# Kernel tuning notes

Measured on AMD Instinct MI355X. Metric: run time of the kernel, lower is better.

The kernel has to match this reference:

```python
import jax, jax.numpy as jnp
import numpy as np

B, L, D = 2, 2048, 4096
H, KV, HD = 32, 8, 128          # query heads, kv heads, head_dim
G = H // KV                      # GQA group size
THETA = 10000.0
SCALE = HD ** -0.5


def apply_rope(x, offset=0):
    """Non-traditional (half-split) RoPE. x: [B, heads, L, HD]."""
    hd = x.shape[-1]
    half = hd // 2
    inv_freq = 1.0 / (THETA ** (jnp.arange(0, hd, 2, dtype=jnp.float32) / hd))  # [half]
    pos = jnp.arange(offset, offset + x.shape[2], dtype=jnp.float32)            # [L]
    ang = pos[:, None] * inv_freq[None, :]                                      # [L, half]
    cos = jnp.cos(ang).astype(x.dtype)
    sin = jnp.sin(ang).astype(x.dtype)
    x1, x2 = x[..., :half], x[..., half:]
    return jnp.concatenate([x1 * cos - x2 * sin, x2 * cos + x1 * sin], axis=-1)


def setup_inputs() -> dict:
    key = jax.random.key(0)
    ks = jax.random.split(key, 8)
    s = 0.02
    return {
        "x": jax.random.normal(ks[0], (B, L, D), dtype=jnp.float32),
        "Wq": jax.random.normal(ks[1], (D, H * HD), dtype=jnp.float32) * s,
        "bq": jnp.zeros((H * HD,), dtype=jnp.float32),
        "Wk": jax.random.normal(ks[2], (D, KV * HD), dtype=jnp.float32) * s,
        "bk": jnp.zeros((KV * HD,), dtype=jnp.float32),
        "Wv": jax.random.normal(ks[3], (D, KV * HD), dtype=jnp.float32) * s,
        "bv": jnp.zeros((KV * HD,), dtype=jnp.float32),
        "Wo": jax.random.normal(ks[4], (H * HD, D), dtype=jnp.float32) * s,
    }


def reference(x, Wq, bq, Wk, bk, Wv, bv, Wo):
    b, l, _ = x.shape
    # projections
    q = (x @ Wq + bq).reshape(b, l, H, HD).transpose(0, 2, 1, 3)   # [B,H,L,HD]
    k = (x @ Wk + bk).reshape(b, l, KV, HD).transpose(0, 2, 1, 3)  # [B,KV,L,HD]
    v = (x @ Wv + bv).reshape(b, l, KV, HD).transpose(0, 2, 1, 3)  # [B,KV,L,HD]
    # RoPE (cache=None path, offset 0)
    q = apply_rope(q)
    k = apply_rope(k)
    # GQA SDPA without materializing repeated KV heads
    qg = q.reshape(b, KV, G, l, HD)                                 # [B,KV,G,L,HD]
    scores = jnp.einsum('bkgld,bkmd->bkglm', qg, k) * SCALE         # [B,KV,G,L,L]
    probs = jax.nn.softmax(scores, axis=-1)
    out = jnp.einsum('bkglm,bkmd->bkgld', probs, v)                 # [B,KV,G,L,HD]
    out = out.reshape(b, H, l, HD).transpose(0, 2, 1, 3).reshape(b, l, H * HD)
    return out @ Wo
```

## Files before the change

kernel.cpp:

```cpp
#include <hip/hip_runtime.h>
#include <stdint.h>
#include <stddef.h>


typedef _Float16 half_t;
typedef __attribute__((ext_vector_type(4))) _Float16 f16x4;
typedef __attribute__((ext_vector_type(8))) _Float16 f16x8;
typedef __attribute__((ext_vector_type(4))) float f32x4;

#define NB 2
#define NL 2048
#define ND 4096
#define NH 32
#define NKV 8
#define NHD 128
#define NG 4
#define NQKV 6144
#define QK_SCALE 0.08838834764831845f
#define RLOG2E 1.4426950408889634f
#define M0 6.0f
#define THR 8.0f

static __device__ __forceinline__ void gll16(const void* g, void* l) {
  __builtin_amdgcn_global_load_lds(
      (__attribute__((address_space(1))) void*)(void*)(g),
      (__attribute__((address_space(3))) void*)(l),
      16, 0, 0);
}

__global__ void convert_f32_f16_kernel(const float* __restrict__ in,
                                       half_t* __restrict__ out, int n4) {
  int i = blockIdx.x * 256 + threadIdx.x;
  if (i >= n4) return;
  const float4 v = reinterpret_cast<const float4*>(in)[i];
  f16x4 o;
  o[0] = (half_t)v.x; o[1] = (half_t)v.y; o[2] = (half_t)v.z; o[3] = (half_t)v.w;
  reinterpret_cast<f16x4*>(out)[i] = o;
}

__global__ void wtrans_kernel(const float* __restrict__ W,
                              half_t* __restrict__ Wt, int K, int N) {
  __shared__ float tile[32][33];
  const int n0 = blockIdx.x * 32;
  const int k0 = blockIdx.y * 32;
  const int tx = threadIdx.x, ty = threadIdx.y;
#pragma unroll
  for (int r = 0; r < 32; r += 8)
    tile[ty + r][tx] = W[(size_t)(k0 + ty + r) * N + n0 + tx];
  __syncthreads();
#pragma unroll
  for (int r = 0; r < 32; r += 8)
    Wt[(size_t)(n0 + ty + r) * K + k0 + tx] = (half_t)tile[tx][ty + r];
}

template <typename OutT>
__global__ __launch_bounds__(512, 2) void gemm256_kernel(
    const half_t* __restrict__ A, const half_t* __restrict__ Bt,
    const float* __restrict__ B0, const float* __restrict__ B1,
    const float* __restrict__ B2, OutT* __restrict__ C,
    int M, int N, int K) {
  constexpr int BK = 32;
  __shared__ __align__(16) half_t As[4][256 * BK];
  __shared__ __align__(16) half_t Bs[4][256 * BK];

  const int tid = threadIdx.x;
  const int wave = tid >> 6, lane = tid & 63;
  const int r16 = lane & 15, quad = lane >> 4;
  const int wm = wave >> 2, wn = wave & 3;

  const int nbx = N >> 8;
  const int lid = (int)(blockIdx.y * gridDim.x + blockIdx.x);
  const int nwg = (int)(gridDim.x * gridDim.y);
  const int cpx = nwg >> 3;
  const int swz = (lid & 7) * cpx + (lid >> 3);
  const int brow = (swz / nbx) * 256;
  const int bcol = (swz % nbx) * 256;

  const int NT = K >> 5;

  auto stageA = [&](int t) {
    const int buf = t & 3;
    const int k0 = t << 5;
#pragma unroll
    for (int j = 0; j < 2; ++j) {
      const int s = j * 512 + wave * 64 + lane;
      const int row = s >> 2;
      const int cg = (s & 3) ^ (row & 3);
      gll16(A + (size_t)(brow + row) * K + k0 + cg * 8,
            &As[buf][(j * 512 + wave * 64) * 8]);
    }
  };
  auto stageB = [&](int t) {
    const int buf = t & 3;
    const int k0 = t << 5;
#pragma unroll
    for (int j = 0; j < 2; ++j) {
      const int s = j * 512 + wave * 64 + lane;
      const int row = s >> 2;
      const int cg = (s & 3) ^ (row & 3);
      gll16(Bt + (size_t)(bcol + row) * K + k0 + cg * 8,
            &Bs[buf][(j * 512 + wave * 64) * 8]);
    }
  };

  f32x4 acc[8][4] = {};
  const int csw = (quad ^ (r16 & 3)) << 3;

  stageA(0); stageB(0); stageA(1); stageB(1); stageA(2); stageB(2);
  asm volatile("s_waitcnt vmcnt(8)" ::: "memory");
  __builtin_amdgcn_s_barrier();

  for (int t = 0; t < NT; ++t) {
    const int buf = t & 3;
    const half_t* Ab = &As[buf][0];
    const half_t* Bb = &Bs[buf][0];

    f16x8 af[4], bf[4];
#pragma unroll
    for (int ni = 0; ni < 4; ++ni)
      bf[ni] = *reinterpret_cast<const f16x8*>(
          &Bb[(wn * 64 + ni * 16 + r16) * BK + csw]);
#pragma unroll
    for (int mi = 0; mi < 4; ++mi)
      af[mi] = *reinterpret_cast<const f16x8*>(
          &Ab[(wm * 128 + mi * 16 + r16) * BK + csw]);
    if (t + 3 < NT) stageA(t + 3);
    __builtin_amdgcn_sched_barrier(0);
    __builtin_amdgcn_s_barrier();
    asm volatile("s_waitcnt lgkmcnt(0)" ::: "memory");
    __builtin_amdgcn_sched_barrier(0);
    __builtin_amdgcn_s_setprio(1);
#pragma unroll
    for (int mi = 0; mi < 4; ++mi)
#pragma unroll
      for (int ni = 0; ni < 4; ++ni)
        acc[mi][ni] = __builtin_amdgcn_mfma_f32_16x16x32_f16(
            af[mi], bf[ni], acc[mi][ni], 0, 0, 0);
    __builtin_amdgcn_s_setprio(0);
    __builtin_amdgcn_s_barrier();

    f16x8 ah[4];
#pragma unroll
    for (int mi = 0; mi < 4; ++mi)
      ah[mi] = *reinterpret_cast<const f16x8*>(
          &Ab[(wm * 128 + 64 + mi * 16 + r16) * BK + csw]);
    if (t + 3 < NT) stageB(t + 3);
    if (t + 3 < NT) {
      asm volatile("s_waitcnt vmcnt(8)" ::: "memory");
    } else if (t + 2 < NT) {
      asm volatile("s_waitcnt vmcnt(4)" ::: "memory");
    } else if (t + 1 < NT) {
      asm volatile("s_waitcnt vmcnt(0)" ::: "memory");
    }
    __builtin_amdgcn_sched_barrier(0);
    __builtin_amdgcn_s_barrier();
    asm volatile("s_waitcnt lgkmcnt(0)" ::: "memory");
    __builtin_amdgcn_sched_barrier(0);
    __builtin_amdgcn_s_setprio(1);
#pragma unroll
    for (int mi = 0; mi < 4; ++mi)
#pragma unroll
      for (int ni = 0; ni < 4; ++ni)
        acc[mi + 4][ni] = __builtin_amdgcn_mfma_f32_16x16x32_f16(
            ah[mi], bf[ni], acc[mi + 4][ni], 0, 0, 0);
    __builtin_amdgcn_s_setprio(0);
    __builtin_amdgcn_s_barrier();
  }

#pragma unroll
  for (int ni = 0; ni < 4; ++ni) {
    const int col = bcol + wn * 64 + ni * 16 + r16;
    float bv = 0.0f;
    if (B0) bv = (col < ND) ? B0[col]
                            : (col < ND + NKV * NHD ? B1[col - ND]
                                                    : B2[col - ND - NKV * NHD]);
#pragma unroll
    for (int mi = 0; mi < 8; ++mi) {
      const int row0 = brow + wm * 128 + mi * 16 + quad * 4;
#pragma unroll
      for (int i = 0; i < 4; ++i)
        C[(size_t)(row0 + i) * N + col] = (OutT)(acc[mi][ni][i] + bv);
    }
  }
}

__global__ void ropepack_kernel(const half_t* __restrict__ rawh,
                                half_t* __restrict__ qb,
                                half_t* __restrict__ kb) {
  const size_t idx = (size_t)blockIdx.x * 256 + threadIdx.x;
  const int d = (int)(idx & 63);
  size_t t = idx >> 6;
  const int hp = (int)(t % (NH + NKV)); t /= (NH + NKV);
  const int l = (int)(t % NL);
  const int b = (int)(t / NL);
  const bool isQ = hp < NH;
  const int col0 = isQ ? hp * NHD : ND + (hp - NH) * NHD;
  const half_t* src = rawh + ((size_t)b * NL + l) * NQKV + col0;
  const float x1 = (float)src[d];
  const float x2 = (float)src[d + 64];
  const float inv_freq = exp2f(-(float)d * 0.20762050593045935f);
  const float ang = (float)l * inv_freq;
  float sn, cs;
  __sincosf(ang, &sn, &cs);
  const float scale = isQ ? QK_SCALE : 1.0f;
  half_t* dst = isQ ? qb + ((size_t)(b * NH + hp) * NL + l) * NHD
                    : kb + ((size_t)(b * NKV + (hp - NH)) * NL + l) * NHD;
  dst[d]      = (half_t)((x1 * cs - x2 * sn) * scale);
  dst[d + 64] = (half_t)((x2 * cs + x1 * sn) * scale);
}

__global__ void vtrans16_kernel(const half_t* __restrict__ rawh,
                                half_t* __restrict__ Vt) {
  __shared__ half_t tile[32][34];
  const int bkv = blockIdx.z;
  const int l0 = blockIdx.x * 32;
  const int d0 = blockIdx.y * 32;
  const int b = bkv / NKV, kvh = bkv % NKV;
  const int tx = threadIdx.x, ty = threadIdx.y;
#pragma unroll
  for (int r = 0; r < 32; r += 8)
    tile[ty + r][tx] = rawh[(size_t)(b * NL + l0 + ty + r) * NQKV
                            + ND + NKV * NHD + kvh * NHD + d0 + tx];
  __syncthreads();
  half_t* dst = Vt + (size_t)bkv * NHD * NL;
#pragma unroll
  for (int r = 0; r < 32; r += 8)
    dst[(size_t)(d0 + ty + r) * NL + l0 + tx] = tile[tx][ty + r];
}

#define KVB 64

__global__ __launch_bounds__(512, 2) void attn_kernel(
    const half_t* __restrict__ Q,
    const half_t* __restrict__ Kh,
    const half_t* __restrict__ Vt,
    half_t* __restrict__ O) {
  __shared__ half_t Ks[2][KVB * NHD];
  __shared__ half_t Vs[2][NHD * KVB];
  __shared__ half_t Ps[8][16 * 64];

  const int tid = threadIdx.x;
  const int wave = tid >> 6, lane = tid & 63;
  const int r16 = lane & 15, quad = lane >> 4;
  const int r7 = r16 & 7;

  const int bid = (int)blockIdx.x;
  const int swz = (bid & 7) * 64 + (bid >> 3);
  const int nqt = NL / 256;
  const int bh = swz / nqt, qt = swz % nqt;
  const int b = bh / NH, h = bh % NH;
  const int kvh = h / NG;

  const int qrow0 = qt * 256 + wave * 32;
  const half_t* Qb = Q  + ((size_t)(b * NH + h) * NL + qrow0) * NHD;
  const half_t* Kb = Kh + ((size_t)(b * NKV + kvh) * NL) * NHD;
  const half_t* Vb = Vt + ((size_t)(b * NKV + kvh) * NHD) * NL;
  half_t* Pw = &Ps[wave][0];

  auto stage = [&](int buf, int n0) {
#pragma unroll
    for (int j = 0; j < 2; ++j) {
      const int slot = j * 512 + wave * 64 + lane;
      {
        const int row = slot >> 4;
        const int c = (slot & 15) ^ (row & 7);
        gll16(Kb + (size_t)(n0 + row) * NHD + c * 8,
              &Ks[buf][(j * 512 + wave * 64) * 8]);
      }
      {
        const int row = slot >> 3;
        const int c = (slot & 7) ^ (row & 7);
        gll16(Vb + (size_t)row * NL + n0 + c * 8,
              &Vs[buf][(j * 512 + wave * 64) * 8]);
      }
    }
  };

  stage(0, 0);

  f16x8 qf[2][4];
#pragma unroll
  for (int rt = 0; rt < 2; ++rt)
#pragma unroll
    for (int c = 0; c < 4; ++c)
      qf[rt][c] = *reinterpret_cast<const f16x8*>(
          &Qb[(size_t)(rt * 16 + r16) * NHD + c * 32 + quad * 8]);

  f32x4 oacc[2][8];
  float m_run[2][4], lsum[2][4];
#pragma unroll
  for (int rt = 0; rt < 2; ++rt) {
#pragma unroll
    for (int i = 0; i < 4; ++i) { m_run[rt][i] = M0; lsum[rt][i] = 0.0f; }
#pragma unroll
    for (int dt = 0; dt < 8; ++dt) oacc[rt][dt] = (f32x4){0.f, 0.f, 0.f, 0.f};
  }

  const int swzread = r7 ^ ((r16 >> 3) * 5);

  asm volatile("s_waitcnt vmcnt(0)" ::: "memory");
  __syncthreads();

  int cur = 0;
  for (int t = 0; t < NL / KVB; ++t, cur ^= 1) {
    if (t + 1 < NL / KVB) stage(cur ^ 1, (t + 1) * KVB);

    const half_t* Kc = &Ks[cur][0];
    const half_t* Vc = &Vs[cur][0];

    f32x4 s[2][4] = {};
#pragma unroll
    for (int c = 0; c < 4; ++c) {
      const int ch = ((c * 4 + quad) ^ r7) * 8;
#pragma unroll
      for (int nt = 0; nt < 4; ++nt) {
        f16x8 kf = *reinterpret_cast<const f16x8*>(&Kc[(nt * 16 + r16) * NHD + ch]);
        s[0][nt] = __builtin_amdgcn_mfma_f32_16x16x32_f16(qf[0][c], kf, s[0][nt], 0, 0, 0);
        s[1][nt] = __builtin_amdgcn_mfma_f32_16x16x32_f16(qf[1][c], kf, s[1][nt], 0, 0, 0);
      }
    }

    float mx[2][4];
    bool need = false;
#pragma unroll
    for (int rt = 0; rt < 2; ++rt)
#pragma unroll
      for (int i = 0; i < 4; ++i) {
        mx[rt][i] = fmaxf(fmaxf(s[rt][0][i], s[rt][1][i]),
                          fmaxf(s[rt][2][i], s[rt][3][i]));
        need = need || (mx[rt][i] > m_run[rt][i] + THR);
      }
    if (__any(need ? 1 : 0)) {
#pragma unroll
      for (int rt = 0; rt < 2; ++rt)
#pragma unroll
        for (int i = 0; i < 4; ++i) {
          float m = mx[rt][i];
#pragma unroll
          for (int off = 1; off < 16; off <<= 1)
            m = fmaxf(m, __shfl_xor(m, off));
          const float mn = fmaxf(m_run[rt][i], m);
          const float corr = exp2f((m_run[rt][i] - mn) * RLOG2E);
          m_run[rt][i] = mn;
          lsum[rt][i] *= corr;
#pragma unroll
          for (int dt = 0; dt < 8; ++dt) oacc[rt][dt][i] *= corr;
        }
    }

    f16x8 pa[2][2];
#pragma unroll
    for (int rt = 0; rt < 2; ++rt) {
#pragma unroll
      for (int i = 0; i < 4; ++i) {
        const float mrl = m_run[rt][i] * RLOG2E;
        float p[4];
#pragma unroll
        for (int nt = 0; nt < 4; ++nt)
          p[nt] = exp2f(s[rt][nt][i] * RLOG2E - mrl);
        lsum[rt][i] += (p[0] + p[1]) + (p[2] + p[3]);
        const int row = quad * 4 + i;
        const int swzr = (row & 7) ^ ((row >> 3) * 5);
#pragma unroll
        for (int nt = 0; nt < 4; ++nt)
          Pw[row * 64 + (((nt * 2 + (r16 >> 3)) ^ swzr) * 8) + r7] = (half_t)p[nt];
      }
      pa[rt][0] = *reinterpret_cast<const f16x8*>(&Pw[r16 * 64 + ((quad ^ swzread) * 8)]);
      pa[rt][1] = *reinterpret_cast<const f16x8*>(&Pw[r16 * 64 + (((4 + quad) ^ swzread) * 8)]);
    }

    const int ch0 = (quad ^ r7) * 8;
    const int ch1 = ((4 + quad) ^ r7) * 8;
#pragma unroll
    for (int dt = 0; dt < 8; ++dt) {
      const int row = dt * 16 + r16;
      f16x8 v0 = *reinterpret_cast<const f16x8*>(&Vc[row * 64 + ch0]);
      f16x8 v1 = *reinterpret_cast<const f16x8*>(&Vc[row * 64 + ch1]);
      oacc[0][dt] = __builtin_amdgcn_mfma_f32_16x16x32_f16(pa[0][0], v0, oacc[0][dt], 0, 0, 0);
      oacc[0][dt] = __builtin_amdgcn_mfma_f32_16x16x32_f16(pa[0][1], v1, oacc[0][dt], 0, 0, 0);
      oacc[1][dt] = __builtin_amdgcn_mfma_f32_16x16x32_f16(pa[1][0], v0, oacc[1][dt], 0, 0, 0);
      oacc[1][dt] = __builtin_amdgcn_mfma_f32_16x16x32_f16(pa[1][1], v1, oacc[1][dt], 0, 0, 0);
    }

    asm volatile("s_waitcnt vmcnt(0)" ::: "memory");
    __syncthreads();
  }

  half_t* Ob = O + ((size_t)(b * NL) + qrow0) * (NH * NHD) + (size_t)h * NHD;
#pragma unroll
  for (int rt = 0; rt < 2; ++rt)
#pragma unroll
    for (int i = 0; i < 4; ++i) {
      float l = lsum[rt][i];
#pragma unroll
      for (int off = 1; off < 16; off <<= 1)
        l += __shfl_xor(l, off);
      const float inv = 1.0f / l;
      const int rl = rt * 16 + quad * 4 + i;
#pragma unroll
      for (int dt = 0; dt < 8; ++dt)
        Ob[(size_t)rl * (NH * NHD) + dt * 16 + r16] =
            (half_t)(oacc[rt][dt][i] * inv);
    }
}

extern "C" void kernel_launch(void* const* d_in, const int* in_sizes, int n_in,
                              void* d_out, int out_size, void* d_ws, size_t ws_size,
                              hipStream_t stream) {
  const float* x  = (const float*)d_in[0];
  const float* Wq = (const float*)d_in[1];
  const float* bq = (const float*)d_in[2];
  const float* Wk = (const float*)d_in[3];
  const float* bk = (const float*)d_in[4];
  const float* Wv = (const float*)d_in[5];
  const float* bv = (const float*)d_in[6];
  const float* Wo = (const float*)d_in[7];
  float* out = (float*)d_out;

  char* ws = (char*)d_ws;
  size_t off = 0;
  auto alloc = [&](size_t bytes) {
    size_t cur = off;
    off += (bytes + 255) & ~(size_t)255;
    return cur;
  };
  const size_t M = (size_t)NB * NL;
  half_t* xb   = (half_t*)(ws + alloc(M * ND * 2));
  half_t* wqkv = (half_t*)(ws + alloc((size_t)NQKV * ND * 2));
  half_t* rawh = (half_t*)(ws + alloc(M * NQKV * 2));
  half_t* qb   = (half_t*)(ws + alloc(M * (size_t)(NH * NHD) * 2));
  half_t* kb   = (half_t*)(ws + alloc(M * (size_t)(NKV * NHD) * 2));
  half_t* vt   = (half_t*)(ws + alloc(M * (size_t)(NKV * NHD) * 2));

  {
    int n4 = (int)(M * ND / 4);
    convert_f32_f16_kernel<<<dim3((n4 + 255) / 256), dim3(256), 0, stream>>>(x, xb, n4);
  }
  wtrans_kernel<<<dim3(ND / 32, ND / 32), dim3(32, 8), 0, stream>>>(
      Wq, wqkv, ND, ND);
  wtrans_kernel<<<dim3((NKV * NHD) / 32, ND / 32), dim3(32, 8), 0, stream>>>(
      Wk, wqkv + (size_t)ND * ND, ND, NKV * NHD);
  wtrans_kernel<<<dim3((NKV * NHD) / 32, ND / 32), dim3(32, 8), 0, stream>>>(
      Wv, wqkv + (size_t)(ND + NKV * NHD) * ND, ND, NKV * NHD);

  gemm256_kernel<half_t><<<dim3(NQKV / 256, M / 256), dim3(512), 0, stream>>>(
      xb, wqkv, bq, bk, bv, rawh, (int)M, NQKV, ND);

  ropepack_kernel<<<dim3((unsigned)(M * (NH + NKV) * 64 / 256)), dim3(256), 0, stream>>>(
      rawh, qb, kb);
  vtrans16_kernel<<<dim3(NL / 32, NHD / 32, NB * NKV), dim3(32, 8), 0, stream>>>(rawh, vt);

  wtrans_kernel<<<dim3(ND / 32, ND / 32), dim3(32, 8), 0, stream>>>(Wo, wqkv, NH * NHD, ND);

  attn_kernel<<<dim3(NB * NH * (NL / 256)), dim3(512), 0, stream>>>(qb, kb, vt, xb);

  gemm256_kernel<float><<<dim3(ND / 256, M / 256), dim3(512), 0, stream>>>(
      xb, wqkv, nullptr, nullptr, nullptr, out, (int)M, ND, ND);
}
```

Measured before the change: 685.4 us.

## Collapse GEMM main loop into single-barrier phase with all fragments loaded up front

Restructures the GEMM K-loop from two half-phases, each with its own barriers, setprio and staged loads, into one phase per tile. Each phase waits on vmcnt, issues a single barrier, prefetches both A and B for tile t+3, loads all eight A fragments, then runs 32 MFMAs. This removes three of the four barriers per iteration and the priority toggling, but loses the fine interleaving of LDS reads, global issue and MFMA. It also raises register pressure because eight A fragments are held live at once.

```diff
diff --git a/kernel.cpp b/kernel.cpp
--- a/kernel.cpp
+++ b/kernel.cpp
@@ -107,64 +107,39 @@
   const int csw = (quad ^ (r16 & 3)) << 3;
 
   stageA(0); stageB(0); stageA(1); stageB(1); stageA(2); stageB(2);
-  asm volatile("s_waitcnt vmcnt(8)" ::: "memory");
-  __builtin_amdgcn_s_barrier();
 
   for (int t = 0; t < NT; ++t) {
+    if (t + 3 <= NT) {
+      asm volatile("s_waitcnt vmcnt(8)" ::: "memory");
+    } else if (t + 2 <= NT) {
+      asm volatile("s_waitcnt vmcnt(4)" ::: "memory");
+    } else {
+      asm volatile("s_waitcnt vmcnt(0)" ::: "memory");
+    }
+    __builtin_amdgcn_s_barrier();
+    __builtin_amdgcn_sched_barrier(0);
+
+    if (t + 3 < NT) { stageA(t + 3); stageB(t + 3); }
+
     const int buf = t & 3;
     const half_t* Ab = &As[buf][0];
     const half_t* Bb = &Bs[buf][0];
 
-    f16x8 af[4], bf[4];
+    f16x8 bf[4], af[8];
 #pragma unroll
     for (int ni = 0; ni < 4; ++ni)
       bf[ni] = *reinterpret_cast<const f16x8*>(
           &Bb[(wn * 64 + ni * 16 + r16) * BK + csw]);
 #pragma unroll
-    for (int mi = 0; mi < 4; ++mi)
+    for (int mi = 0; mi < 8; ++mi)
       af[mi] = *reinterpret_cast<const f16x8*>(
           &Ab[(wm * 128 + mi * 16 + r16) * BK + csw]);
-    if (t + 3 < NT) stageA(t + 3);
-    __builtin_amdgcn_sched_barrier(0);
-    __builtin_amdgcn_s_barrier();
-    asm volatile("s_waitcnt lgkmcnt(0)" ::: "memory");
-    __builtin_amdgcn_sched_barrier(0);
-    __builtin_amdgcn_s_setprio(1);
-#pragma unroll
-    for (int mi = 0; mi < 4; ++mi)
+#pragma unroll
+    for (int mi = 0; mi < 8; ++mi)
 #pragma unroll
       for (int ni = 0; ni < 4; ++ni)
         acc[mi][ni] = __builtin_amdgcn_mfma_f32_16x16x32_f16(
             af[mi], bf[ni], acc[mi][ni], 0, 0, 0);
-    __builtin_amdgcn_s_setprio(0);
-    __builtin_amdgcn_s_barrier();
-
-    f16x8 ah[4];
-#pragma unroll
-    for (int mi = 0; mi < 4; ++mi)
-      ah[mi] = *reinterpret_cast<const f16x8*>(
-          &Ab[(wm * 128 + 64 + mi * 16 + r16) * BK + csw]);
-    if (t + 3 < NT) stageB(t + 3);
-    if (t + 3 < NT) {
-      asm volatile("s_waitcnt vmcnt(8)" ::: "memory");
-    } else if (t + 2 < NT) {
-      asm volatile("s_waitcnt vmcnt(4)" ::: "memory");
-    } else if (t + 1 < NT) {
-      asm volatile("s_waitcnt vmcnt(0)" ::: "memory");
-    }
-    __builtin_amdgcn_sched_barrier(0);
-    __builtin_amdgcn_s_barrier();
-    asm volatile("s_waitcnt lgkmcnt(0)" ::: "memory");
-    __builtin_amdgcn_sched_barrier(0);
-    __builtin_amdgcn_s_setprio(1);
-#pragma unroll
-    for (int mi = 0; mi < 4; ++mi)
-#pragma unroll
-      for (int ni = 0; ni < 4; ++ni)
-        acc[mi + 4][ni] = __builtin_amdgcn_mfma_f32_16x16x32_f16(
-            ah[mi], bf[ni], acc[mi + 4][ni], 0, 0, 0);
-    __builtin_amdgcn_s_setprio(0);
-    __builtin_amdgcn_s_barrier();
   }
 
 #pragma unroll
```

Measured after the change: 783.4 us. 14.3% more time.
